# Kernel tuning notes

Hardware: AMD Instinct MI355X
Metric: run time of the kernel (lower is better)

Reference implementation:

```python
import jax, jax.numpy as jnp
import numpy as np

C = 8.0  # RG-LRU temporal-gate constant (Griffin paper, c = 8)


def setup_inputs() -> dict:
    key = jax.random.key(0)
    ks = jax.random.split(key, 4)
    S, B, D = 2048, 8, 2048  # (seq_len, batch, width); batch_first=False layout
    s = 1.0 / np.sqrt(D).astype(np.float32)
    return {
        "x": jax.random.normal(ks[0], (S, B, D), jnp.float32),
        "h0": jnp.zeros((B, D), jnp.float32),
        "W_x": jax.random.normal(ks[1], (D, D), jnp.float32) * s,
        "b_x": jnp.zeros((D,), jnp.float32),
        "W_a": jax.random.normal(ks[2], (D, D), jnp.float32) * s,
        "b_a": jnp.zeros((D,), jnp.float32),
        "a_param": jax.random.uniform(ks[3], (D,), jnp.float32, 0.3, 1.0),
    }


def _rg_lru(x, h0, W_x, b_x, W_a, b_a, a_param):
    # x: (S, B, D) time-major. RG-LRU (Griffin/Hawk), num_heads=1 so the
    # block-diagonal gate projections are plain dense D->D linears.
    S = x.shape[0]
    gate_x = jax.nn.sigmoid(jnp.einsum("sbd,ed->sbe", x, W_x) + b_x)  # input gate
    gate_a = jax.nn.sigmoid(jnp.einsum("sbd,ed->sbe", x, W_a) + b_a)  # recurrence gate
    log_a = -C * gate_a * jax.nn.softplus(a_param)  # (S, B, D), log of decay in (0,1)
    a = jnp.exp(log_a)
    multiplier = jnp.sqrt(1.0 - jnp.exp(2.0 * log_a))  # sqrt(1 - a^2) normalizer
    # Reset at segment start (t == 0): multiplier -> 1, decay -> 0 (cache cleared).
    reset = (jnp.arange(S) == 0)[:, None, None]
    multiplier = jnp.where(reset, 1.0, multiplier)
    a = jnp.where(reset, 0.0, a)
    normed_x = x * gate_x * multiplier  # gated, variance-normalized input

    def step(h, inp):
        a_t, x_t = inp
        h = a_t * h + x_t  # diagonal linear recurrence
        return h, h

    hn, y = jax.lax.scan(step, h0, (a, normed_x))
    return y, hn  # y: (S, B, D) since batch_first=False; hn: (B, D)


def reference(x, h0, W_x, b_x, W_a, b_a, a_param):
    return _rg_lru(x, h0, W_x, b_x, W_a, b_a, a_param)
```

## Files before the change

### kernel.cpp

```cpp
#include <hip/hip_runtime.h>
#include <cstdint>

#define S_LEN 2048
#define B_SZ 8
#define D_DIM 2048
#define M_DIM (S_LEN * B_SZ)
#define CHAINS (B_SZ * D_DIM)
#define BK 64
#define KTILES (D_DIM / BK)

typedef __bf16 bf16;
typedef bf16 bf16x8 __attribute__((ext_vector_type(8)));
typedef bf16 bf16x4 __attribute__((ext_vector_type(4)));
typedef float f32x4 __attribute__((ext_vector_type(4)));

__device__ __forceinline__ void async_copy16(void* lds, const void* g) {
    __builtin_amdgcn_global_load_lds(
        (const __attribute__((address_space(1))) unsigned int*)g,
        (__attribute__((address_space(3))) unsigned int*)lds,
        16, 0, 0);
}

__device__ __forceinline__ unsigned short bf16_bits(float f) {
    bf16 b = (bf16)f;
    return __builtin_bit_cast(unsigned short, b);
}

__global__ void k_convert(const float4* __restrict__ x,
                          const float4* __restrict__ wx,
                          const float4* __restrict__ wa,
                          bf16* __restrict__ xb,
                          bf16* __restrict__ wi) {
    const long NX4 = (long)M_DIM * D_DIM / 4;
    const long NW4 = (long)D_DIM * D_DIM / 4;
    const long total = NX4 + 2 * NW4;
    for (long i = (long)blockIdx.x * blockDim.x + threadIdx.x; i < total;
         i += (long)gridDim.x * blockDim.x) {
        float4 v;
        bf16* dst;
        if (i < NX4) {
            v = x[i];
            dst = xb + 4 * i;
        } else {
            long k = i - NX4;
            const int isA = k >= NW4;
            if (isA) k -= NW4;
            const long e = k >> 9;
            const long col4 = k & 511;
            const long drow = (e >> 4) * 32 + (isA ? 16 : 0) + (e & 15);
            v = (isA ? wa : wx)[k];
            dst = wi + (drow * 512 + col4) * 4;
        }
        bf16x4 o;
        o[0] = (bf16)v.x; o[1] = (bf16)v.y; o[2] = (bf16)v.z; o[3] = (bf16)v.w;
        *reinterpret_cast<bf16x4*>(dst) = o;
    }
}

__global__ void k_cvec(const float* __restrict__ ap, float* __restrict__ cv) {
    int e = blockIdx.x * blockDim.x + threadIdx.x;
    if (e < D_DIM) {
        float v = ap[e];
        cv[e] = -8.0f * log1pf(expf(v));
    }
}

__global__ __launch_bounds__(512, 2) void k_gemm(
    const bf16* __restrict__ xb,
    const bf16* __restrict__ wi,
    const float* __restrict__ bx,
    const float* __restrict__ ba,
    const float* __restrict__ cv,
    unsigned int* __restrict__ pk)
{
    __shared__ __align__(16) char smem[131072];

    const int tid  = threadIdx.x;
    const int lane = tid & 63;
    const int w    = tid >> 6;
    const int wm   = w >> 2;
    const int wn   = w & 3;

    const int orig = blockIdx.x;
    const int wgid = (orig & 7) * 128 + (orig >> 3);
    const int m0 = (wgid & 63) * 256;
    const int e0 = (wgid >> 6) * 256;

    const int srow  = lane >> 3;
    const int swz16 = ((lane & 7) ^ srow) * 16;

    const char* gA = (const char*)xb;
    const char* gB = (const char*)wi;

#define STAGE_A(buf, kt) do {                                                  \
    const long kb_ = (long)(kt) * 128 + swz16;                                 \
    _Pragma("unroll")                                                          \
    for (int j_ = 0; j_ < 4; ++j_) {                                           \
        const int br_ = w * 32 + j_ * 8;                                       \
        async_copy16(smem + (buf) * 65536 + br_ * 128,                         \
                     gA + ((long)(m0 + br_ + srow) * 4096 + kb_));             \
    } } while (0)

#define STAGE_B(buf, kt) do {                                                  \
    const long kb_ = (long)(kt) * 128 + swz16;                                 \
    _Pragma("unroll")                                                          \
    for (int j_ = 0; j_ < 4; ++j_) {                                           \
        const int br_ = w * 32 + j_ * 8;                                       \
        async_copy16(smem + (buf) * 65536 + 32768 + br_ * 128,                 \
                     gB + ((long)(e0 + br_ + srow) * 4096 + kb_));             \
    } } while (0)

#define PHASE_GO() do {                                                        \
    asm volatile("s_waitcnt lgkmcnt(0)" ::: "memory");                         \
    __builtin_amdgcn_sched_barrier(0);                                         \
    __builtin_amdgcn_s_setprio(1); } while (0)
#define PHASE_DONE() __builtin_amdgcn_s_setprio(0)

    f32x4 acc[8][4];
#pragma unroll
    for (int i = 0; i < 8; ++i)
#pragma unroll
        for (int j = 0; j < 4; ++j) acc[i][j] = (f32x4)(0.0f);

    STAGE_A(0, 0); STAGE_B(0, 0);
    asm volatile("s_waitcnt vmcnt(0)" ::: "memory");
    __builtin_amdgcn_s_barrier();

    const int rL = lane & 15;

    for (int kt = 0; kt < KTILES; ++kt) {
        const int c  = kt & 1;
        const int nb = 1 - c;
        char* sA = smem + c * 65536;
        char* sB = sA + 32768;
        const bool pf = (kt < KTILES - 1);

        bf16x8 af[4], bf[4];

#define LOAD_AF(ihalf, ks) do {                                                \
    _Pragma("unroll")                                                          \
    for (int i_ = 0; i_ < 4; ++i_) {                                           \
        const int r_ = wm * 128 + ((ihalf) * 4 + i_) * 16 + rL;                \
        const int ch_ = (((ks) * 4 + (lane >> 4)) ^ (r_ & 7)) * 16;            \
        af[i_] = *reinterpret_cast<const bf16x8*>(sA + r_ * 128 + ch_);        \
    } } while (0)

#define LOAD_BF(ks) do {                                                       \
    _Pragma("unroll")                                                          \
    for (int j_ = 0; j_ < 4; ++j_) {                                           \
        const int r_ = wn * 64 + j_ * 16 + rL;                                 \
        const int ch_ = (((ks) * 4 + (lane >> 4)) ^ (r_ & 7)) * 16;            \
        bf[j_] = *reinterpret_cast<const bf16x8*>(sB + r_ * 128 + ch_);        \
    } } while (0)

#define MFMA16(ihalf) do {                                                     \
    _Pragma("unroll")                                                          \
    for (int i_ = 0; i_ < 4; ++i_)                                             \
        _Pragma("unroll")                                                      \
        for (int j_ = 0; j_ < 4; ++j_)                                         \
            acc[(ihalf) * 4 + i_][j_] = __builtin_amdgcn_mfma_f32_16x16x32_bf16( \
                af[i_], bf[j_], acc[(ihalf) * 4 + i_][j_], 0, 0, 0);           \
    } while (0)

        LOAD_BF(0); LOAD_AF(0, 0);
        if (pf) STAGE_A(nb, kt + 1);
        PHASE_GO(); MFMA16(0); PHASE_DONE();

        LOAD_AF(1, 0);
        if (pf) STAGE_B(nb, kt + 1);
        PHASE_GO(); MFMA16(1); PHASE_DONE();

        LOAD_BF(1); LOAD_AF(0, 1);
        PHASE_GO(); MFMA16(0); PHASE_DONE();

        LOAD_AF(1, 1);
        PHASE_GO(); MFMA16(1); PHASE_DONE();

        if (pf) asm volatile("s_waitcnt vmcnt(0)" ::: "memory");
        __builtin_amdgcn_s_barrier();

#undef LOAD_AF
#undef LOAD_BF
#undef MFMA16
    }

#undef STAGE_A
#undef STAGE_B
#undef PHASE_GO
#undef PHASE_DONE

    const int rgrp = lane >> 4;
    const int chb  = (e0 + wn * 64) >> 1;
#pragma unroll
    for (int jj = 0; jj < 2; ++jj) {
        const int ch = chb + jj * 16 + rL;
        const float bxv = bx[ch];
        const float bav = ba[ch];
        const float cvv = cv[ch];
#pragma unroll
        for (int i = 0; i < 8; ++i) {
#pragma unroll
            for (int r = 0; r < 4; ++r) {
                const int m = m0 + wm * 128 + i * 16 + rgrp * 4 + r;
                const float zx = acc[i][2 * jj][r] + bxv;
                const float za = acc[i][2 * jj + 1][r] + bav;
                const float gx = 1.0f / (1.0f + __expf(-zx));
                const float ga = 1.0f / (1.0f + __expf(-za));
                float la = cvv * ga;
                float mult = sqrtf(fmaxf(1.0f - __expf(2.0f * la), 0.0f));
                if (m < B_SZ) { la = -100.0f; mult = 1.0f; }
                const long o = (long)m * D_DIM + ch;
                const float xv = (float)xb[o];
                const float xn = xv * gx * mult;
                const unsigned int u =
                    ((unsigned int)bf16_bits(xn) << 16) | bf16_bits(la);
                pk[o] = u;
            }
        }
    }
}

__global__ __launch_bounds__(64) void k_scan(
    const unsigned int* __restrict__ pk,
    float* __restrict__ y,
    const float* __restrict__ h0,
    float* __restrict__ hn) {
    const int c = blockIdx.x * 64 + threadIdx.x;
    float h = h0[c];

    unsigned int u0[16], u1[16];
#pragma unroll
    for (int j = 0; j < 16; ++j) u0[j] = pk[(long)j * CHAINS + c];

    for (int g = 0; g < 128; g += 2) {
        const long base1 = ((long)(g + 1) * 16) * CHAINS + c;
        if (g + 1 < 128) {
#pragma unroll
            for (int j = 0; j < 16; ++j) u1[j] = pk[base1 + (long)j * CHAINS];
        }
        const long base0 = ((long)g * 16) * CHAINS + c;
#pragma unroll
        for (int j = 0; j < 16; ++j) {
            const unsigned int u = u0[j];
            const float la = __builtin_bit_cast(float, u << 16);
            const float xn = __builtin_bit_cast(float, u & 0xffff0000u);
            h = fmaf(__expf(la), h, xn);
            y[base0 + (long)j * CHAINS] = h;
        }
        const long base2 = ((long)(g + 2) * 16) * CHAINS + c;
        if (g + 2 < 128) {
#pragma unroll
            for (int j = 0; j < 16; ++j) u0[j] = pk[base2 + (long)j * CHAINS];
        }
        if (g + 1 < 128) {
#pragma unroll
            for (int j = 0; j < 16; ++j) {
                const unsigned int u = u1[j];
                const float la = __builtin_bit_cast(float, u << 16);
                const float xn = __builtin_bit_cast(float, u & 0xffff0000u);
                h = fmaf(__expf(la), h, xn);
                y[base1 + (long)j * CHAINS] = h;
            }
        }
    }
    hn[c] = h;
}

extern "C" void kernel_launch(void* const* d_in, const int* in_sizes, int n_in,
                              void* d_out, int out_size, void* d_ws, size_t ws_size,
                              hipStream_t stream) {
    const float* x  = (const float*)d_in[0];
    const float* h0 = (const float*)d_in[1];
    const float* Wx = (const float*)d_in[2];
    const float* bx = (const float*)d_in[3];
    const float* Wa = (const float*)d_in[4];
    const float* ba = (const float*)d_in[5];
    const float* ap = (const float*)d_in[6];
    float* out = (float*)d_out;

    char* ws = (char*)d_ws;
    bf16*  xb = (bf16*)(ws);
    bf16*  wi = (bf16*)(ws + 67108864L);
    float* cv = (float*)(ws + 83886080L);
    unsigned int* pk = (unsigned int*)(ws + 83894272L);

    float* y  = out;
    float* hn = out + (long)M_DIM * D_DIM;

    k_convert<<<dim3(2048), dim3(256), 0, stream>>>(
        (const float4*)x, (const float4*)Wx, (const float4*)Wa, xb, wi);
    k_cvec<<<dim3(8), dim3(256), 0, stream>>>(ap, cv);
    k_gemm<<<dim3((M_DIM / 256) * (2 * D_DIM / 256)), dim3(512), 0, stream>>>(
        xb, wi, bx, ba, cv, pk);
    k_scan<<<dim3(CHAINS / 64), dim3(64), 0, stream>>>(pk, y, h0, hn);
}
```

Measured before the change: 418.1 us.

## Split K-tile staging into halves with new LDS swizzle and finer waits

Stores each 64-wide K tile in LDS as two 32-column halves of 64-byte rows with a new XOR/rotate swizzle. Loads for the next tile are issued in four half-tile groups spread across the MFMA phases. Partial vmcnt(4) waits plus a mid-iteration barrier let compute on the second half overlap the loads still in flight. This adds an extra barrier per iteration, and the new swizzle must remain bank-conflict free for both the async writes and the fragment reads.

```diff
diff --git a/kernel.cpp b/kernel.cpp
--- a/kernel.cpp
+++ b/kernel.cpp
@@ -86,28 +86,30 @@
     const int m0 = (wgid & 63) * 256;
     const int e0 = (wgid >> 6) * 256;
 
-    const int srow  = lane >> 3;
-    const int swz16 = ((lane & 7) ^ srow) * 16;
+    const int rw   = lane >> 2;
+    const int cw16 = (((lane & 3) ^ ((lane >> 2) & 3)) - (lane >> 4) & 3) * 16;
+    const int lcr16 = (((((lane >> 4) + ((lane >> 2) & 3)) & 3) ^ (lane & 3)) * 16);
+    const int rL = lane & 15;
 
     const char* gA = (const char*)xb;
     const char* gB = (const char*)wi;
 
-#define STAGE_A(buf, kt) do {                                                  \
-    const long kb_ = (long)(kt) * 128 + swz16;                                 \
-    _Pragma("unroll")                                                          \
-    for (int j_ = 0; j_ < 4; ++j_) {                                           \
-        const int br_ = w * 32 + j_ * 8;                                       \
-        async_copy16(smem + (buf) * 65536 + br_ * 128,                         \
-                     gA + ((long)(m0 + br_ + srow) * 4096 + kb_));             \
+#define STAGE_A(buf, kt, kh) do {                                              \
+    _Pragma("unroll")                                                          \
+    for (int j_ = 0; j_ < 2; ++j_) {                                           \
+        const int rb_ = w * 32 + j_ * 16;                                      \
+        async_copy16(smem + (buf) * 65536 + (kh) * 16384 + rb_ * 64,           \
+                     gA + ((long)(m0 + rb_ + rw) * 4096 +                      \
+                           (long)(kt) * 128 + (kh) * 64 + cw16));              \
     } } while (0)
 
-#define STAGE_B(buf, kt) do {                                                  \
-    const long kb_ = (long)(kt) * 128 + swz16;                                 \
-    _Pragma("unroll")                                                          \
-    for (int j_ = 0; j_ < 4; ++j_) {                                           \
-        const int br_ = w * 32 + j_ * 8;                                       \
-        async_copy16(smem + (buf) * 65536 + 32768 + br_ * 128,                 \
-                     gB + ((long)(e0 + br_ + srow) * 4096 + kb_));             \
+#define STAGE_B(buf, kt, kh) do {                                              \
+    _Pragma("unroll")                                                          \
+    for (int j_ = 0; j_ < 2; ++j_) {                                           \
+        const int rb_ = w * 32 + j_ * 16;                                      \
+        async_copy16(smem + (buf) * 65536 + 32768 + (kh) * 16384 + rb_ * 64,   \
+                     gB + ((long)(e0 + rb_ + rw) * 4096 +                      \
+                           (long)(kt) * 128 + (kh) * 64 + cw16));              \
     } } while (0)
 
 #define PHASE_GO() do {                                                        \
@@ -122,11 +124,9 @@
 #pragma unroll
         for (int j = 0; j < 4; ++j) acc[i][j] = (f32x4)(0.0f);
 
-    STAGE_A(0, 0); STAGE_B(0, 0);
-    asm volatile("s_waitcnt vmcnt(0)" ::: "memory");
+    STAGE_A(0, 0, 0); STAGE_B(0, 0, 0); STAGE_A(0, 0, 1); STAGE_B(0, 0, 1);
+    asm volatile("s_waitcnt vmcnt(4)" ::: "memory");
     __builtin_amdgcn_s_barrier();
-
-    const int rL = lane & 15;
 
     for (int kt = 0; kt < KTILES; ++kt) {
         const int c  = kt & 1;
@@ -141,16 +141,16 @@
     _Pragma("unroll")                                                          \
     for (int i_ = 0; i_ < 4; ++i_) {                                           \
         const int r_ = wm * 128 + ((ihalf) * 4 + i_) * 16 + rL;                \
-        const int ch_ = (((ks) * 4 + (lane >> 4)) ^ (r_ & 7)) * 16;            \
-        af[i_] = *reinterpret_cast<const bf16x8*>(sA + r_ * 128 + ch_);        \
+        af[i_] = *reinterpret_cast<const bf16x8*>(                             \
+            sA + (ks) * 16384 + r_ * 64 + lcr16);                              \
     } } while (0)
 
 #define LOAD_BF(ks) do {                                                       \
     _Pragma("unroll")                                                          \
     for (int j_ = 0; j_ < 4; ++j_) {                                           \
         const int r_ = wn * 64 + j_ * 16 + rL;                                 \
-        const int ch_ = (((ks) * 4 + (lane >> 4)) ^ (r_ & 7)) * 16;            \
-        bf[j_] = *reinterpret_cast<const bf16x8*>(sB + r_ * 128 + ch_);        \
+        bf[j_] = *reinterpret_cast<const bf16x8*>(                             \
+            sB + (ks) * 16384 + r_ * 64 + lcr16);                              \
     } } while (0)
 
 #define MFMA16(ihalf) do {                                                     \
@@ -163,21 +163,29 @@
     } while (0)
 
         LOAD_BF(0); LOAD_AF(0, 0);
-        if (pf) STAGE_A(nb, kt + 1);
+        if (pf) STAGE_A(nb, kt + 1, 0);
         PHASE_GO(); MFMA16(0); PHASE_DONE();
 
         LOAD_AF(1, 0);
-        if (pf) STAGE_B(nb, kt + 1);
+        if (pf) STAGE_B(nb, kt + 1, 0);
         PHASE_GO(); MFMA16(1); PHASE_DONE();
 
+        if (pf) asm volatile("s_waitcnt vmcnt(4)" ::: "memory");
+        else    asm volatile("s_waitcnt vmcnt(0)" ::: "memory");
+        __builtin_amdgcn_s_barrier();
+
         LOAD_BF(1); LOAD_AF(0, 1);
+        if (pf) STAGE_A(nb, kt + 1, 1);
         PHASE_GO(); MFMA16(0); PHASE_DONE();
 
         LOAD_AF(1, 1);
+        if (pf) STAGE_B(nb, kt + 1, 1);
         PHASE_GO(); MFMA16(1); PHASE_DONE();
 
-        if (pf) asm volatile("s_waitcnt vmcnt(0)" ::: "memory");
-        __builtin_amdgcn_s_barrier();
+        if (pf) {
+            asm volatile("s_waitcnt vmcnt(4)" ::: "memory");
+            __builtin_amdgcn_s_barrier();
+        }
 
 #undef LOAD_AF
 #undef LOAD_BF
```

Measured after the change: 437.0 us. 1.05x slower.

## Split tile staging into per-row-group chunks and relax vmcnt waits across phases

Applied to the files above, without the earlier changes.

Global-to-LDS staging of the next K tile is broken into row-group units and spread across all four MFMA phases instead of being issued in two bursts. The end-of-iteration wait becomes vmcnt(2), leaving the last A chunks in flight. A new wait and barrier after the first phase make sure those chunks land before the rows that need them are read. This aims to keep more memory traffic overlapped with compute, at the cost of an extra barrier per iteration and tighter correctness reasoning about which rows are ready.

```diff
diff --git a/kernel.cpp b/kernel.cpp
--- a/kernel.cpp
+++ b/kernel.cpp
@@ -92,23 +92,19 @@
     const char* gA = (const char*)xb;
     const char* gB = (const char*)wi;
 
-#define STAGE_A(buf, kt) do {                                                  \
-    const long kb_ = (long)(kt) * 128 + swz16;                                 \
-    _Pragma("unroll")                                                          \
-    for (int j_ = 0; j_ < 4; ++j_) {                                           \
-        const int br_ = w * 32 + j_ * 8;                                       \
-        async_copy16(smem + (buf) * 65536 + br_ * 128,                         \
-                     gA + ((long)(m0 + br_ + srow) * 4096 + kb_));             \
-    } } while (0)
-
-#define STAGE_B(buf, kt) do {                                                  \
-    const long kb_ = (long)(kt) * 128 + swz16;                                 \
-    _Pragma("unroll")                                                          \
-    for (int j_ = 0; j_ < 4; ++j_) {                                           \
-        const int br_ = w * 32 + j_ * 8;                                       \
-        async_copy16(smem + (buf) * 65536 + 32768 + br_ * 128,                 \
-                     gB + ((long)(e0 + br_ + srow) * 4096 + kb_));             \
-    } } while (0)
+#define SU_A(buf, kt, u) do {                                                  \
+    const int rb_ = (u) * 64 + w * 8;                                          \
+    async_copy16(smem + (buf) * 65536 + rb_ * 128,                             \
+                 gA + ((long)(m0 + rb_ + srow) * 4096 +                        \
+                       (long)(kt) * 128 + swz16));                             \
+    } while (0)
+
+#define SU_B(buf, kt, u) do {                                                  \
+    const int rb_ = (u) * 64 + w * 8;                                          \
+    async_copy16(smem + (buf) * 65536 + 32768 + rb_ * 128,                     \
+                 gB + ((long)(e0 + rb_ + srow) * 4096 +                        \
+                       (long)(kt) * 128 + swz16));                             \
+    } while (0)
 
 #define PHASE_GO() do {                                                        \
     asm volatile("s_waitcnt lgkmcnt(0)" ::: "memory");                         \
@@ -122,8 +118,10 @@
 #pragma unroll
         for (int j = 0; j < 4; ++j) acc[i][j] = (f32x4)(0.0f);
 
-    STAGE_A(0, 0); STAGE_B(0, 0);
-    asm volatile("s_waitcnt vmcnt(0)" ::: "memory");
+    SU_A(0, 0, 0); SU_A(0, 0, 2);
+    SU_B(0, 0, 0); SU_B(0, 0, 1); SU_B(0, 0, 2); SU_B(0, 0, 3);
+    SU_A(0, 0, 1); SU_A(0, 0, 3);
+    asm volatile("s_waitcnt vmcnt(2)" ::: "memory");
     __builtin_amdgcn_s_barrier();
 
     const int rL = lane & 15;
@@ -163,29 +161,36 @@
     } while (0)
 
         LOAD_BF(0); LOAD_AF(0, 0);
-        if (pf) STAGE_A(nb, kt + 1);
+        if (pf) { SU_A(nb, kt + 1, 0); SU_A(nb, kt + 1, 2); }
         PHASE_GO(); MFMA16(0); PHASE_DONE();
+        if (pf) asm volatile("s_waitcnt vmcnt(2)" ::: "memory");
+        else    asm volatile("s_waitcnt vmcnt(0)" ::: "memory");
+        __builtin_amdgcn_s_barrier();
 
         LOAD_AF(1, 0);
-        if (pf) STAGE_B(nb, kt + 1);
+        if (pf) { SU_B(nb, kt + 1, 0); SU_B(nb, kt + 1, 1); }
         PHASE_GO(); MFMA16(1); PHASE_DONE();
 
         LOAD_BF(1); LOAD_AF(0, 1);
+        if (pf) { SU_B(nb, kt + 1, 2); SU_B(nb, kt + 1, 3); }
         PHASE_GO(); MFMA16(0); PHASE_DONE();
 
         LOAD_AF(1, 1);
+        if (pf) { SU_A(nb, kt + 1, 1); SU_A(nb, kt + 1, 3); }
         PHASE_GO(); MFMA16(1); PHASE_DONE();
 
-        if (pf) asm volatile("s_waitcnt vmcnt(0)" ::: "memory");
-        __builtin_amdgcn_s_barrier();
+        if (pf) {
+            asm volatile("s_waitcnt vmcnt(2)" ::: "memory");
+            __builtin_amdgcn_s_barrier();
+        }
 
 #undef LOAD_AF
 #undef LOAD_BF
 #undef MFMA16
     }
 
-#undef STAGE_A
-#undef STAGE_B
+#undef SU_A
+#undef SU_B
 #undef PHASE_GO
 #undef PHASE_DONE
 
```

Result: no change. 414.4 us, median of 2 (-0.9%).
